# Optimization experiments

Hardware: AMD Instinct MI355X
Metric: run time of the kernel (lower is better)

## Reference

```python
import jax, jax.numpy as jnp
import numpy as np

B, P, N = 64, 100, 1000
D, H, QD = 128, 8, 16
NUM_GROUPS = 5
MAX_DELTA = 4
SQRT_EMB = float(np.sqrt(D))
CLIP = 10.0
BIAS_INIT = 0.2
BIAS_TAU = 1.0


def setup_inputs() -> dict:
    key = jax.random.key(0)
    ks = jax.random.split(key, 12)
    w_scale = 1.0 / np.sqrt(D)
    encoded_nodes = jax.random.normal(ks[0], (B, N, D), dtype=jnp.float32)
    encoded_q1 = jax.random.normal(ks[1], (B, P, D), dtype=jnp.float32)
    encoded_last_node = jax.random.normal(ks[2], (B, P, D), dtype=jnp.float32)
    ninf_mask = jnp.where(jax.random.uniform(ks[3], (B, P, N)) < 0.2,
                          -jnp.inf, 0.0).astype(jnp.float32)
    Wq_first = (jax.random.normal(ks[4], (D, H * QD)) * w_scale).astype(jnp.float32)
    Wq_last = (jax.random.normal(ks[5], (D, H * QD)) * w_scale).astype(jnp.float32)
    Wk = (jax.random.normal(ks[6], (D, H * QD)) * w_scale).astype(jnp.float32)
    Wv = (jax.random.normal(ks[7], (D, H * QD)) * w_scale).astype(jnp.float32)
    W_comb = (jax.random.normal(ks[8], (H * QD, D)) * w_scale).astype(jnp.float32)
    b_comb = jnp.zeros((D,), dtype=jnp.float32)
    # learnable priority-bias table, init = 0.2 * exp(-delta / tau)
    deltas = jnp.arange(MAX_DELTA + 1, dtype=jnp.float32)
    bias_table = (BIAS_INIT * jnp.exp(-deltas / BIAS_TAU)).astype(jnp.float32)
    group_ids = jax.random.randint(ks[10], (B, N), 0, NUM_GROUPS).astype(jnp.int32)
    current_min_priority = jax.random.randint(ks[11], (B, P), 0, NUM_GROUPS).astype(jnp.int32)
    return {
        'encoded_nodes': encoded_nodes, 'encoded_q1': encoded_q1,
        'encoded_last_node': encoded_last_node, 'ninf_mask': ninf_mask,
        'Wq_first': Wq_first, 'Wq_last': Wq_last, 'Wk': Wk, 'Wv': Wv,
        'W_comb': W_comb, 'b_comb': b_comb, 'bias_table': bias_table,
        'group_ids': group_ids, 'current_min_priority': current_min_priority,
    }


def _heads(x):
    # [B, n, H*QD] -> [B, H, n, QD]
    b, n, _ = x.shape
    return x.reshape(b, n, H, QD).transpose(0, 2, 1, 3)


def reference(encoded_nodes, encoded_q1, encoded_last_node, ninf_mask,
              Wq_first, Wq_last, Wk, Wv, W_comb, b_comb, bias_table,
              group_ids, current_min_priority):
    # set_kv / set_q1
    k = _heads(encoded_nodes @ Wk)            # [B,H,N,QD]
    v = _heads(encoded_nodes @ Wv)            # [B,H,N,QD]
    q_first = _heads(encoded_q1 @ Wq_first)   # [B,H,P,QD]
    # forward
    q_last = _heads(encoded_last_node @ Wq_last)
    q = q_first + q_last
    score = jnp.einsum('bhpd,bhnd->bhpn', q, k) / jnp.sqrt(jnp.float32(QD))
    score = score + ninf_mask[:, None, :, :]  # rank3 ninf mask
    weights = jax.nn.softmax(score, axis=-1)
    out = jnp.einsum('bhpn,bhnd->bhpd', weights, v)
    out_concat = out.transpose(0, 2, 1, 3).reshape(B, P, H * QD)
    mh_atten_out = out_concat @ W_comb + b_comb  # [B,P,D]
    # single-head score against encoder embeddings
    score2 = jnp.einsum('bpd,bnd->bpn', mh_atten_out, encoded_nodes) / SQRT_EMB
    score_clipped = CLIP * jnp.tanh(score2)
    # relative-priority bias gather
    delta = jnp.clip(group_ids[:, None, :] - current_min_priority[:, :, None],
                     0, MAX_DELTA)                     # [B,P,N] int
    priority_bias = bias_table[delta]                  # gather
    priority_bias = jnp.where(jnp.isfinite(ninf_mask), priority_bias, 0.0)
    score_masked = score_clipped + priority_bias + ninf_mask
    probs = jax.nn.softmax(score_masked, axis=-1)
    return probs
```

## Files before the change

### kernel.cpp

```cpp
#include <hip/hip_runtime.h>

#define BB 64
#define PP 100
#define NN 1000
#define DDIM 128
#define HH 8
#define NSPL 8

typedef __attribute__((ext_vector_type(8))) short bf16x8;
typedef __attribute__((ext_vector_type(16))) float f32x16;
typedef __attribute__((ext_vector_type(4))) unsigned u32x4;
typedef __attribute__((ext_vector_type(2))) unsigned u32x2;

__device__ __forceinline__ unsigned bf16rne(float x) {
  unsigned u = __float_as_uint(x);
  return (u + 0x7FFFu + ((u >> 16) & 1u)) >> 16;
}
__device__ __forceinline__ unsigned pk_bf16(float a, float b) {
  return bf16rne(a) | (bf16rne(b) << 16);
}

__device__ __forceinline__ void split8(const float* __restrict__ p,
                                       bf16x8& hi8, bf16x8& lo8) {
  const float4 a = *(const float4*)p;
  const float4 c = *(const float4*)(p + 4);
  float v[8] = {a.x, a.y, a.z, a.w, c.x, c.y, c.z, c.w};
  unsigned hw[4], lw[4];
#pragma unroll
  for (int j = 0; j < 4; ++j) {
    const unsigned h0 = bf16rne(v[2*j]), h1 = bf16rne(v[2*j+1]);
    hw[j] = h0 | (h1 << 16);
    lw[j] = bf16rne(v[2*j]   - __uint_as_float(h0 << 16)) |
            (bf16rne(v[2*j+1] - __uint_as_float(h1 << 16)) << 16);
  }
  hi8 = __builtin_bit_cast(bf16x8, u32x4{hw[0], hw[1], hw[2], hw[3]});
  lo8 = __builtin_bit_cast(bf16x8, u32x4{lw[0], lw[1], lw[2], lw[3]});
}

__global__ __launch_bounds__(256) void pack_w_kernel(
    const float* __restrict__ W0, const float* __restrict__ W1,
    const float* __restrict__ W2, const float* __restrict__ W3,
    const float* __restrict__ W4, u32x4* __restrict__ wfrag)
{
  const int gid = blockIdx.x * 256 + threadIdx.x;
  const int mat = gid >> 11;
  const int ct = (gid >> 9) & 3;
  const int ks = (gid >> 6) & 7;
  const int lane = gid & 63;
  const float* __restrict__ W =
      (mat == 0) ? W0 : (mat == 1) ? W1 : (mat == 2) ? W2 : (mat == 3) ? W3 : W4;
  const int col = ct * 32 + (lane & 31);
  const int k0 = ks * 16 + (lane >> 5) * 8;
  unsigned hi[4], lo[4];
#pragma unroll
  for (int j = 0; j < 4; ++j) {
    const float x0 = W[(k0 + 2 * j) * DDIM + col];
    const float x1 = W[(k0 + 2 * j + 1) * DDIM + col];
    const unsigned h0 = bf16rne(x0), h1 = bf16rne(x1);
    hi[j] = h0 | (h1 << 16);
    lo[j] = bf16rne(x0 - __uint_as_float(h0 << 16)) |
            (bf16rne(x1 - __uint_as_float(h1 << 16)) << 16);
  }
  const int base = (((mat * 4 + ct) * 8 + ks) * 2) * 64 + lane;
  wfrag[base]      = u32x4{hi[0], hi[1], hi[2], hi[3]};
  wfrag[base + 64] = u32x4{lo[0], lo[1], lo[2], lo[3]};
}

__global__ __launch_bounds__(256) void proj_kv_mfma_kernel(
    const float* __restrict__ x, const u32x4* __restrict__ wfrag,
    float* __restrict__ outk, float* __restrict__ outv)
{
  const int tid = threadIdx.x;
  const int lane = tid & 63;
  const int wid = tid >> 6;
  const int rtp = wid >> 1;
  const int ctp = wid & 1;
  const int arow = blockIdx.x * 128 + rtp * 64 + (lane & 31);
  const int kgrp = (lane >> 5) * 8;

#pragma unroll 1
  for (int mat = 0; mat < 2; ++mat) {
    float* __restrict__ out = mat ? outv : outk;
    f32x16 acc[2][2];
#pragma unroll
    for (int a = 0; a < 2; ++a)
#pragma unroll
      for (int b = 0; b < 2; ++b)
#pragma unroll
        for (int i = 0; i < 16; ++i) acc[a][b][i] = 0.f;

#pragma unroll 1
    for (int ks = 0; ks < 8; ++ks) {
      bf16x8 ahi[2], alo[2];
#pragma unroll
      for (int rt = 0; rt < 2; ++rt) {
        const float* xp = x + (size_t)(arow + rt * 32) * DDIM + ks * 16 + kgrp;
        split8(xp, ahi[rt], alo[rt]);
      }
#pragma unroll
      for (int ct = 0; ct < 2; ++ct) {
        const int c = ctp * 2 + ct;
        const int fo = (((mat * 4 + c) * 8 + ks) * 2) * 64 + lane;
        const bf16x8 bhi = __builtin_bit_cast(bf16x8, wfrag[fo]);
        const bf16x8 blo = __builtin_bit_cast(bf16x8, wfrag[fo + 64]);
#pragma unroll
        for (int rt = 0; rt < 2; ++rt) {
          acc[rt][ct] = __builtin_amdgcn_mfma_f32_32x32x16_bf16(
              ahi[rt], bhi, acc[rt][ct], 0, 0, 0);
          acc[rt][ct] = __builtin_amdgcn_mfma_f32_32x32x16_bf16(
              ahi[rt], blo, acc[rt][ct], 0, 0, 0);
          acc[rt][ct] = __builtin_amdgcn_mfma_f32_32x32x16_bf16(
              alo[rt], bhi, acc[rt][ct], 0, 0, 0);
        }
      }
    }
#pragma unroll
    for (int rt = 0; rt < 2; ++rt)
#pragma unroll
      for (int ct = 0; ct < 2; ++ct) {
        const int colg = ctp * 64 + ct * 32 + (lane & 31);
        const int rowg0 = blockIdx.x * 128 + rtp * 64 + rt * 32 + 4 * (lane >> 5);
#pragma unroll
        for (int r = 0; r < 16; ++r) {
          const int rowg = rowg0 + (r & 3) + 8 * (r >> 2);
          out[(size_t)rowg * DDIM + colg] = acc[rt][ct][r];
        }
      }
  }
}

__global__ __launch_bounds__(256) void proj_q2_mfma_kernel(
    const float* __restrict__ x1, const float* __restrict__ x2,
    const u32x4* __restrict__ wfrag, float* __restrict__ out, float scale)
{
  const int tid = threadIdx.x;
  const int lane = tid & 63;
  const int w = tid >> 6;
  const int hi = lane >> 5;
  const int l31 = lane & 31;
  const int row0 = blockIdx.x * 128 + w * 32;
  const float* xr1 = x1 + (size_t)(row0 + l31) * DDIM + hi * 8;
  const float* xr2 = x2 + (size_t)(row0 + l31) * DDIM + hi * 8;

  f32x16 acc[4];
#pragma unroll
  for (int ct = 0; ct < 4; ++ct)
#pragma unroll
    for (int i = 0; i < 16; ++i) acc[ct][i] = 0.f;

#pragma unroll 1
  for (int ks = 0; ks < 8; ++ks) {
    bf16x8 a1h, a1l, a2h, a2l;
    split8(xr1 + ks * 16, a1h, a1l);
    split8(xr2 + ks * 16, a2h, a2l);
#pragma unroll
    for (int ct = 0; ct < 4; ++ct) {
      const int fo1 = (((2 * 4 + ct) * 8 + ks) * 2) * 64 + lane;
      const bf16x8 b1h = __builtin_bit_cast(bf16x8, wfrag[fo1]);
      const bf16x8 b1l = __builtin_bit_cast(bf16x8, wfrag[fo1 + 64]);
      acc[ct] = __builtin_amdgcn_mfma_f32_32x32x16_bf16(a1h, b1h, acc[ct], 0, 0, 0);
      acc[ct] = __builtin_amdgcn_mfma_f32_32x32x16_bf16(a1h, b1l, acc[ct], 0, 0, 0);
      acc[ct] = __builtin_amdgcn_mfma_f32_32x32x16_bf16(a1l, b1h, acc[ct], 0, 0, 0);
      const int fo2 = (((3 * 4 + ct) * 8 + ks) * 2) * 64 + lane;
      const bf16x8 b2h = __builtin_bit_cast(bf16x8, wfrag[fo2]);
      const bf16x8 b2l = __builtin_bit_cast(bf16x8, wfrag[fo2 + 64]);
      acc[ct] = __builtin_amdgcn_mfma_f32_32x32x16_bf16(a2h, b2h, acc[ct], 0, 0, 0);
      acc[ct] = __builtin_amdgcn_mfma_f32_32x32x16_bf16(a2h, b2l, acc[ct], 0, 0, 0);
      acc[ct] = __builtin_amdgcn_mfma_f32_32x32x16_bf16(a2l, b2h, acc[ct], 0, 0, 0);
    }
  }
#pragma unroll
  for (int ct = 0; ct < 4; ++ct) {
    const int colg = ct * 32 + l31;
    const int rowg0 = row0 + 4 * hi;
#pragma unroll
    for (int r = 0; r < 16; ++r) {
      const int rowg = rowg0 + (r & 3) + 8 * (r >> 2);
      out[(size_t)rowg * DDIM + colg] = acc[ct][r] * scale;
    }
  }
}

__global__ __launch_bounds__(256) void proj_comb_mfma_kernel(
    const float* __restrict__ x, const u32x4* __restrict__ wfrag,
    const float* __restrict__ bias, float* __restrict__ out)
{
  const int tid = threadIdx.x;
  const int lane = tid & 63;
  const int w = tid >> 6;
  const int hi = lane >> 5;
  const int l31 = lane & 31;
  const int row0 = blockIdx.x * 128 + w * 32;
  const float* xr = x + (size_t)(row0 + l31) * DDIM + hi * 8;

  f32x16 acc[4];
#pragma unroll
  for (int ct = 0; ct < 4; ++ct)
#pragma unroll
    for (int i = 0; i < 16; ++i) acc[ct][i] = 0.f;

#pragma unroll 1
  for (int ks = 0; ks < 8; ++ks) {
    bf16x8 ah, al;
    split8(xr + ks * 16, ah, al);
#pragma unroll
    for (int ct = 0; ct < 4; ++ct) {
      const int fo = (((4 * 4 + ct) * 8 + ks) * 2) * 64 + lane;
      const bf16x8 bh = __builtin_bit_cast(bf16x8, wfrag[fo]);
      const bf16x8 bl = __builtin_bit_cast(bf16x8, wfrag[fo + 64]);
      acc[ct] = __builtin_amdgcn_mfma_f32_32x32x16_bf16(ah, bh, acc[ct], 0, 0, 0);
      acc[ct] = __builtin_amdgcn_mfma_f32_32x32x16_bf16(ah, bl, acc[ct], 0, 0, 0);
      acc[ct] = __builtin_amdgcn_mfma_f32_32x32x16_bf16(al, bh, acc[ct], 0, 0, 0);
    }
  }
#pragma unroll
  for (int ct = 0; ct < 4; ++ct) {
    const int colg = ct * 32 + l31;
    const float bj = bias[colg];
    const int rowg0 = row0 + 4 * hi;
#pragma unroll
    for (int r = 0; r < 16; ++r) {
      const int rowg = rowg0 + (r & 3) + 8 * (r >> 2);
      out[(size_t)rowg * DDIM + colg] = acc[ct][r] + bj;
    }
  }
}

__global__ __launch_bounds__(512) void attn_mfma_kernel(
    const float* __restrict__ Q, const float* __restrict__ K,
    const float* __restrict__ V, const float* __restrict__ mask,
    float* __restrict__ po, float* __restrict__ lsum)
{
  __shared__ float mask_lds[PP * 132];

  const int b = blockIdx.x >> 3;
  const int chunk = blockIdx.x & 7;
  const int n0 = chunk * 128;
  const int tid = threadIdx.x;
  const int h = tid >> 6;
  const int l = tid & 63;
  const int hi = l >> 5;
  const int l31 = l & 31;

  const float NINF = -__builtin_huge_valf();
  for (int idx = tid; idx < PP * 32; idx += 512) {
    const int p = idx >> 5;
    const int c = idx & 31;
    const int nb4 = n0 + 4 * c;
    const int nsrc = min(nb4, NN - 4);
    float4 f = *(const float4*)(mask + ((size_t)(b * PP + p)) * NN + nsrc);
    f.x = (nb4 + 0 < NN) ? f.x : NINF;
    f.y = (nb4 + 1 < NN) ? f.y : NINF;
    f.z = (nb4 + 2 < NN) ? f.z : NINF;
    f.w = (nb4 + 3 < NN) ? f.w : NINF;
    *(float4*)&mask_lds[p * 132 + 4 * c] = f;
  }
  __syncthreads();

  bf16x8 qhi[4], qlo[4];
#pragma unroll
  for (int pt = 0; pt < 4; ++pt) {
    const int qrow = min(b * PP + pt * 32 + l31, BB * PP - 1);
    split8(Q + (size_t)qrow * DDIM + h * 16 + hi * 8, qhi[pt], qlo[pt]);
  }

  f32x16 oacc[4];
#pragma unroll
  for (int pt = 0; pt < 4; ++pt)
#pragma unroll
    for (int i = 0; i < 16; ++i) oacc[pt][i] = 0.f;
  float lacc[4] = {0.f, 0.f, 0.f, 0.f};

  const float* Kb = K + (size_t)b * NN * DDIM + h * 16;
  const float* Vb = V + (size_t)b * NN * DDIM + h * 16;
  const int dv = min(l31, 15);

#pragma unroll 1
  for (int nt = 0; nt < 4; ++nt) {
    const int nb = n0 + nt * 32;

    bf16x8 khi, klo;
    {
      const int krow = min(nb + l31, NN - 1);
      split8(Kb + (size_t)krow * DDIM + hi * 8, khi, klo);
    }
    bf16x8 vhi[2], vlo[2];
#pragma unroll
    for (int ks = 0; ks < 2; ++ks) {
      float vt[8];
#pragma unroll
      for (int i = 0; i < 8; ++i) {
        const int vrow = min(nb + ks * 16 + hi * 8 + i, NN - 1);
        vt[i] = Vb[(size_t)vrow * DDIM + dv];
      }
      unsigned vh[4], vl[4];
#pragma unroll
      for (int j = 0; j < 4; ++j) {
        const unsigned h0 = bf16rne(vt[2*j]), h1 = bf16rne(vt[2*j+1]);
        vh[j] = h0 | (h1 << 16);
        vl[j] = bf16rne(vt[2*j]   - __uint_as_float(h0 << 16)) |
                (bf16rne(vt[2*j+1] - __uint_as_float(h1 << 16)) << 16);
      }
      vhi[ks] = __builtin_bit_cast(bf16x8, u32x4{vh[0], vh[1], vh[2], vh[3]});
      vlo[ks] = __builtin_bit_cast(bf16x8, u32x4{vl[0], vl[1], vl[2], vl[3]});
    }

#pragma unroll
    for (int pt = 0; pt < 4; ++pt) {
      const int prow = min(pt * 32 + l31, PP - 1);
      f32x16 s;
#pragma unroll
      for (int q = 0; q < 4; ++q) {
        const float4 f =
            *(const float4*)&mask_lds[prow * 132 + nt * 32 + q * 8 + hi * 4];
        s[4*q+0] = f.x; s[4*q+1] = f.y; s[4*q+2] = f.z; s[4*q+3] = f.w;
      }
      s = __builtin_amdgcn_mfma_f32_32x32x16_bf16(khi, qhi[pt], s, 0, 0, 0);
      s = __builtin_amdgcn_mfma_f32_32x32x16_bf16(khi, qlo[pt], s, 0, 0, 0);
      s = __builtin_amdgcn_mfma_f32_32x32x16_bf16(klo, qhi[pt], s, 0, 0, 0);

      float ev[16];
#pragma unroll
      for (int r = 0; r < 16; ++r) {
        const float e = __expf(s[r]);
        ev[r] = e;
        lacc[pt] += e;
      }
      unsigned u[8];
#pragma unroll
      for (int j = 0; j < 8; ++j) u[j] = pk_bf16(ev[2*j], ev[2*j+1]);
#pragma unroll
      for (int ks = 0; ks < 2; ++ks) {
        const unsigned t01 = u[ks*4+0], t23 = u[ks*4+1];
        const unsigned t45 = u[ks*4+2], t67 = u[ks*4+3];
        const u32x2 r0 = __builtin_amdgcn_permlane32_swap(t01, t45, false, false);
        const u32x2 r1 = __builtin_amdgcn_permlane32_swap(t23, t67, false, false);
        const bf16x8 pah = __builtin_bit_cast(bf16x8,
            u32x4{r0[0], r1[0], r0[1], r1[1]});
        oacc[pt] = __builtin_amdgcn_mfma_f32_32x32x16_bf16(pah, vhi[ks], oacc[pt], 0, 0, 0);
        oacc[pt] = __builtin_amdgcn_mfma_f32_32x32x16_bf16(pah, vlo[ks], oacc[pt], 0, 0, 0);
      }
    }
  }

  const int base = (b * NSPL + chunk) * PP;
#pragma unroll
  for (int pt = 0; pt < 4; ++pt) {
    const float ltot = lacc[pt] + __shfl_xor(lacc[pt], 32, 64);
    const int pl = pt * 32 + l31;
    if (l < 32 && pl < PP)
      lsum[(size_t)(base + pl) * HH + h] = ltot;
#pragma unroll
    for (int r = 0; r < 16; ++r) {
      const int p = pt * 32 + (r & 3) + 8 * (r >> 2) + 4 * hi;
      if (l31 < 16 && p < PP)
        po[(size_t)(base + p) * DDIM + h * 16 + l31] = oacc[pt][r];
    }
  }
}

__global__ __launch_bounds__(256) void merge_kernel(
    const float* __restrict__ po, const float* __restrict__ lsum,
    float* __restrict__ mh_in)
{
  const int idx = blockIdx.x * 256 + threadIdx.x;
  const int d = idx & 127;
  const int row = idx >> 7;
  const int b = row / PP;
  const int p = row - b * PP;
  const int h = d >> 4;
  float s = 0.f, lt = 0.f;
#pragma unroll
  for (int sp = 0; sp < NSPL; ++sp) {
    const int base = (b * NSPL + sp) * PP + p;
    s  += po[base * DDIM + d];
    lt += lsum[base * HH + h];
  }
  mh_in[idx] = s / lt;
}

__global__ __launch_bounds__(256) void score2_mfma_kernel(
    const float* __restrict__ enc, const float* __restrict__ mh,
    const float* __restrict__ mask, const float* __restrict__ bias_table,
    const int* __restrict__ group_ids, const int* __restrict__ cur_min,
    float* __restrict__ out, float* __restrict__ ssum)
{
  const int b   = blockIdx.x >> 4;
  const int nc  = blockIdx.x & 15;
  const int n0  = nc * 64;
  const int tid = threadIdx.x;
  const int lane = tid & 63;
  const int mt   = tid >> 6;
  const int half = lane >> 5;
  const int l31  = lane & 31;

  f32x16 acc[2];
#pragma unroll
  for (int c = 0; c < 2; ++c)
#pragma unroll
    for (int i = 0; i < 16; ++i) acc[c][i] = 0.f;

  const float* mha = mh + ((size_t)(b * PP + 32 * mt + l31)) * DDIM + half * 8;
  const float* encb = enc + (size_t)b * NN * DDIM + half * 8;
  const int nsrc0 = min(n0 + l31, NN - 1);
  const int nsrc1 = min(n0 + 32 + l31, NN - 1);

#pragma unroll 1
  for (int ks = 0; ks < 8; ++ks) {
    bf16x8 ahi, alo;
    split8(mha + ks * 16, ahi, alo);
    bf16x8 bhi0, blo0, bhi1, blo1;
    split8(encb + (size_t)nsrc0 * DDIM + ks * 16, bhi0, blo0);
    split8(encb + (size_t)nsrc1 * DDIM + ks * 16, bhi1, blo1);
    acc[0] = __builtin_amdgcn_mfma_f32_32x32x16_bf16(ahi, bhi0, acc[0], 0, 0, 0);
    acc[0] = __builtin_amdgcn_mfma_f32_32x32x16_bf16(ahi, blo0, acc[0], 0, 0, 0);
    acc[0] = __builtin_amdgcn_mfma_f32_32x32x16_bf16(alo, bhi0, acc[0], 0, 0, 0);
    acc[1] = __builtin_amdgcn_mfma_f32_32x32x16_bf16(ahi, bhi1, acc[1], 0, 0, 0);
    acc[1] = __builtin_amdgcn_mfma_f32_32x32x16_bf16(ahi, blo1, acc[1], 0, 0, 0);
    acc[1] = __builtin_amdgcn_mfma_f32_32x32x16_bf16(alo, bhi1, acc[1], 0, 0, 0);
  }

  const float t0 = bias_table[0], t1 = bias_table[1], t2 = bias_table[2],
              t3 = bias_table[3], t4 = bias_table[4];
  const float two_inv_sqrt_emb = 0.1767766952966369f;

  float rsum[16];
#pragma unroll
  for (int r = 0; r < 16; ++r) rsum[r] = 0.f;

#pragma unroll
  for (int ct = 0; ct < 2; ++ct) {
    const int n = n0 + ct * 32 + l31;
    const bool nvalid = n < NN;
    const int nr = nvalid ? n : NN - 1;
    const int gid = group_ids[b * NN + nr];
#pragma unroll
    for (int r = 0; r < 16; ++r) {
      const int p = 32 * mt + (r & 3) + 8 * (r >> 2) + 4 * half;
      const bool pvalid = p < PP;
      const int pr = pvalid ? p : PP - 1;
      const float m = mask[((size_t)(b * PP + pr)) * NN + nr];
      const float ex = __expf(acc[ct][r] * two_inv_sqrt_emb);
      const float sc = 10.0f - 20.0f / (ex + 1.0f);
      const int cmp = cur_min[b * PP + pr];
      int delta = gid - cmp;
      delta = delta < 0 ? 0 : (delta > 4 ? 4 : delta);
      const float pb = (delta == 0) ? t0 : (delta == 1) ? t1 : (delta == 2) ? t2
                     : (delta == 3) ? t3 : t4;
      float e = (nvalid && pvalid) ? __expf(sc + pb + m) : 0.0f;
      if (nvalid && pvalid) out[((size_t)(b * PP + p)) * NN + n] = e;
      rsum[r] += e;
    }
  }
#pragma unroll
  for (int r = 0; r < 16; ++r) {
    float ws = rsum[r];
#pragma unroll
    for (int off = 1; off < 32; off <<= 1) ws += __shfl_xor(ws, off, 64);
    rsum[r] = ws;
  }
  if (l31 == 0) {
#pragma unroll
    for (int r = 0; r < 16; ++r) {
      const int p = 32 * mt + (r & 3) + 8 * (r >> 2) + 4 * half;
      if (p < PP) ssum[(size_t)(b * PP + p) * 16 + nc] = rsum[r];
    }
  }
}

__global__ __launch_bounds__(256) void norm_kernel(
    const float* __restrict__ ssum, float* __restrict__ out)
{
  const int row = blockIdx.x;
  float s = 0.f;
#pragma unroll
  for (int i = 0; i < 16; ++i) s += ssum[(size_t)row * 16 + i];
  const float inv = 1.0f / s;
#pragma unroll
  for (int i = 0; i < 4; ++i) {
    const int c = i * 256 + (int)threadIdx.x;
    if (c < NN) out[(size_t)row * NN + c] *= inv;
  }
}

extern "C" void kernel_launch(void* const* d_in, const int* in_sizes, int n_in,
                              void* d_out, int out_size, void* d_ws, size_t ws_size,
                              hipStream_t stream)
{
  (void)in_sizes; (void)n_in; (void)out_size; (void)ws_size;
  const float* enc_nodes  = (const float*)d_in[0];
  const float* enc_q1     = (const float*)d_in[1];
  const float* enc_last   = (const float*)d_in[2];
  const float* ninf       = (const float*)d_in[3];
  const float* Wq_first   = (const float*)d_in[4];
  const float* Wq_last    = (const float*)d_in[5];
  const float* Wk         = (const float*)d_in[6];
  const float* Wv         = (const float*)d_in[7];
  const float* W_comb     = (const float*)d_in[8];
  const float* b_comb     = (const float*)d_in[9];
  const float* bias_table = (const float*)d_in[10];
  const int*   group_ids  = (const int*)d_in[11];
  const int*   cur_min    = (const int*)d_in[12];
  float* out = (float*)d_out;
  float* ws  = (float*)d_ws;

  float* Qw = ws;
  float* Kw = Qw + 819200;
  float* Vw = Kw + 8192000;
  float* po = Vw + 8192000;
  float* ls = po + 6553600;
  float* mh = ls + 409600;
  float* sm = mh + 819200;

  u32x4* wfrag = (u32x4*)sm;

  pack_w_kernel<<<40, 256, 0, stream>>>(Wk, Wv, Wq_first, Wq_last, W_comb, wfrag);
  proj_q2_mfma_kernel<<<BB*PP/128, 256, 0, stream>>>(enc_q1, enc_last, wfrag,
                                                     Qw, 0.25f);
  proj_kv_mfma_kernel<<<BB*NN/128, 256, 0, stream>>>(enc_nodes, wfrag, Kw, Vw);
  attn_mfma_kernel<<<BB*NSPL, 512, 0, stream>>>(Qw, Kw, Vw, ninf, po, ls);
  merge_kernel<<<3200, 256, 0, stream>>>(po, ls, Qw);
  proj_comb_mfma_kernel<<<BB*PP/128, 256, 0, stream>>>(Qw, wfrag, b_comb, mh);
  score2_mfma_kernel<<<BB*16, 256, 0, stream>>>(enc_nodes, mh, ninf, bias_table,
                                                group_ids, cur_min, out, sm);
  norm_kernel<<<BB*PP, 256, 0, stream>>>(sm, out);
}
```

Measured before the change: 177.9 us.

## Pre-pack encoder and mh into bf16 hi/lo MFMA fragments for score2

Adds two packing kernels that convert encoded_nodes and the multi-head output into split bf16 hi/lo fragments laid out in MFMA operand order. They write into the K workspace, which is dead by that point. score2 then reads these fragments with coalesced vector loads instead of doing strided fp32 loads and splitting them in the inner loop. The cur_min loads are also hoisted out of the epilogue loop. The cost is extra kernel launches and an extra pass over the encoder data (read fp32, write twice as many bf16 halves).

```diff
diff --git a/kernel.cpp b/kernel.cpp
--- a/kernel.cpp
+++ b/kernel.cpp
@@ -64,6 +64,38 @@
   const int base = (((mat * 4 + ct) * 8 + ks) * 2) * 64 + lane;
   wfrag[base]      = u32x4{hi[0], hi[1], hi[2], hi[3]};
   wfrag[base + 64] = u32x4{lo[0], lo[1], lo[2], lo[3]};
+}
+
+__global__ __launch_bounds__(512) void pack_enc_kernel(
+    const float* __restrict__ enc, u32x4* __restrict__ encp)
+{
+  const int b = blockIdx.x >> 5;
+  const int t = blockIdx.x & 31;
+  const int ks = threadIdx.x >> 6;
+  const int lane = threadIdx.x & 63;
+  const int n = min(32 * t + (lane & 31), NN - 1);
+  const int k0 = ks * 16 + (lane >> 5) * 8;
+  bf16x8 hi8, lo8;
+  split8(enc + ((size_t)b * NN + n) * DDIM + k0, hi8, lo8);
+  const size_t base = ((size_t)(b * 32 + t) * 8 + ks) * 128 + lane;
+  encp[base]      = __builtin_bit_cast(u32x4, hi8);
+  encp[base + 64] = __builtin_bit_cast(u32x4, lo8);
+}
+
+__global__ __launch_bounds__(512) void pack_mh_kernel(
+    const float* __restrict__ mh, u32x4* __restrict__ mhp)
+{
+  const int b = blockIdx.x >> 2;
+  const int mt = blockIdx.x & 3;
+  const int ks = threadIdx.x >> 6;
+  const int lane = threadIdx.x & 63;
+  const int p = min(32 * mt + (lane & 31), PP - 1);
+  const int k0 = ks * 16 + (lane >> 5) * 8;
+  bf16x8 hi8, lo8;
+  split8(mh + ((size_t)b * PP + p) * DDIM + k0, hi8, lo8);
+  const size_t base = ((size_t)(b * 4 + mt) * 8 + ks) * 128 + lane;
+  mhp[base]      = __builtin_bit_cast(u32x4, hi8);
+  mhp[base + 64] = __builtin_bit_cast(u32x4, lo8);
 }
 
 __global__ __launch_bounds__(256) void proj_kv_mfma_kernel(
@@ -380,7 +412,7 @@
 }
 
 __global__ __launch_bounds__(256) void score2_mfma_kernel(
-    const float* __restrict__ enc, const float* __restrict__ mh,
+    const u32x4* __restrict__ encp, const u32x4* __restrict__ mhp,
     const float* __restrict__ mask, const float* __restrict__ bias_table,
     const int* __restrict__ group_ids, const int* __restrict__ cur_min,
     float* __restrict__ out, float* __restrict__ ssum)
@@ -400,18 +432,18 @@
 #pragma unroll
     for (int i = 0; i < 16; ++i) acc[c][i] = 0.f;
 
-  const float* mha = mh + ((size_t)(b * PP + 32 * mt + l31)) * DDIM + half * 8;
-  const float* encb = enc + (size_t)b * NN * DDIM + half * 8;
-  const int nsrc0 = min(n0 + l31, NN - 1);
-  const int nsrc1 = min(n0 + 32 + l31, NN - 1);
-
-#pragma unroll 1
+  const u32x4* ma  = mhp  + ((size_t)(b * 4 + mt) * 8) * 128 + lane;
+  const u32x4* eb0 = encp + ((size_t)(b * 32 + nc * 2) * 8) * 128 + lane;
+  const u32x4* eb1 = encp + ((size_t)(b * 32 + nc * 2 + 1) * 8) * 128 + lane;
+
+#pragma unroll 2
   for (int ks = 0; ks < 8; ++ks) {
-    bf16x8 ahi, alo;
-    split8(mha + ks * 16, ahi, alo);
-    bf16x8 bhi0, blo0, bhi1, blo1;
-    split8(encb + (size_t)nsrc0 * DDIM + ks * 16, bhi0, blo0);
-    split8(encb + (size_t)nsrc1 * DDIM + ks * 16, bhi1, blo1);
+    const bf16x8 ahi  = __builtin_bit_cast(bf16x8, ma[ks * 128]);
+    const bf16x8 alo  = __builtin_bit_cast(bf16x8, ma[ks * 128 + 64]);
+    const bf16x8 bhi0 = __builtin_bit_cast(bf16x8, eb0[ks * 128]);
+    const bf16x8 blo0 = __builtin_bit_cast(bf16x8, eb0[ks * 128 + 64]);
+    const bf16x8 bhi1 = __builtin_bit_cast(bf16x8, eb1[ks * 128]);
+    const bf16x8 blo1 = __builtin_bit_cast(bf16x8, eb1[ks * 128 + 64]);
     acc[0] = __builtin_amdgcn_mfma_f32_32x32x16_bf16(ahi, bhi0, acc[0], 0, 0, 0);
     acc[0] = __builtin_amdgcn_mfma_f32_32x32x16_bf16(ahi, blo0, acc[0], 0, 0, 0);
     acc[0] = __builtin_amdgcn_mfma_f32_32x32x16_bf16(alo, bhi0, acc[0], 0, 0, 0);
@@ -423,6 +455,13 @@
   const float t0 = bias_table[0], t1 = bias_table[1], t2 = bias_table[2],
               t3 = bias_table[3], t4 = bias_table[4];
   const float two_inv_sqrt_emb = 0.1767766952966369f;
+
+  int cmpv[16];
+#pragma unroll
+  for (int r = 0; r < 16; ++r) {
+    const int p = 32 * mt + (r & 3) + 8 * (r >> 2) + 4 * half;
+    cmpv[r] = cur_min[b * PP + min(p, PP - 1)];
+  }
 
   float rsum[16];
 #pragma unroll
@@ -442,8 +481,7 @@
       const float m = mask[((size_t)(b * PP + pr)) * NN + nr];
       const float ex = __expf(acc[ct][r] * two_inv_sqrt_emb);
       const float sc = 10.0f - 20.0f / (ex + 1.0f);
-      const int cmp = cur_min[b * PP + pr];
-      int delta = gid - cmp;
+      int delta = gid - cmpv[r];
       delta = delta < 0 ? 0 : (delta > 4 ? 4 : delta);
       const float pb = (delta == 0) ? t0 : (delta == 1) ? t1 : (delta == 2) ? t2
                      : (delta == 3) ? t3 : t4;
@@ -513,6 +551,8 @@
   float* sm = mh + 819200;
 
   u32x4* wfrag = (u32x4*)sm;
+  u32x4* encp = (u32x4*)Kw;
+  u32x4* mhp  = ((u32x4*)Kw) + 2097152;
 
   pack_w_kernel<<<40, 256, 0, stream>>>(Wk, Wv, Wq_first, Wq_last, W_comb, wfrag);
   proj_q2_mfma_kernel<<<BB*PP/128, 256, 0, stream>>>(enc_q1, enc_last, wfrag,
@@ -520,8 +560,10 @@
   proj_kv_mfma_kernel<<<BB*NN/128, 256, 0, stream>>>(enc_nodes, wfrag, Kw, Vw);
   attn_mfma_kernel<<<BB*NSPL, 512, 0, stream>>>(Qw, Kw, Vw, ninf, po, ls);
   merge_kernel<<<3200, 256, 0, stream>>>(po, ls, Qw);
+  pack_enc_kernel<<<BB*32, 512, 0, stream>>>(enc_nodes, encp);
   proj_comb_mfma_kernel<<<BB*PP/128, 256, 0, stream>>>(Qw, wfrag, b_comb, mh);
-  score2_mfma_kernel<<<BB*16, 256, 0, stream>>>(enc_nodes, mh, ninf, bias_table,
+  pack_mh_kernel<<<BB*4, 512, 0, stream>>>(mh, mhp);
+  score2_mfma_kernel<<<BB*16, 256, 0, stream>>>(encp, mhp, ninf, bias_table,
                                                 group_ids, cur_min, out, sm);
   norm_kernel<<<BB*PP, 256, 0, stream>>>(sm, out);
 }
```

New measurement: 176.9 us. About the same (-0.6%).
